# Kernel optimization log

Hardware: AMD Instinct MI355X
Metric: run time of the kernel (lower is better)

Reference implementation:

```python
import jax, jax.numpy as jnp
import numpy as np

N_NODES = 50000
N_EDGES = 500000
IN_FEATS = 64
H_FEATS = 128
NUM_CLASSES = 4
NUM_GRAPHS = 8
NODES_PER_GRAPH = N_NODES // NUM_GRAPHS


def setup_inputs() -> dict:
    key = jax.random.key(0)
    ks = jax.random.split(key, 12)
    in_feat = jax.random.normal(ks[0], (N_NODES, IN_FEATS), dtype=jnp.float32)
    e_weight = jax.random.uniform(ks[1], (N_EDGES,), dtype=jnp.float32)
    src = jax.random.randint(ks[2], (N_EDGES,), 0, N_NODES)
    dst = jax.random.randint(ks[3], (N_EDGES,), 0, N_NODES)
    batch_num_nodes = jnp.full((NUM_GRAPHS,), NODES_PER_GRAPH, dtype=jnp.int64)
    target_node = jax.random.randint(ks[4], (NUM_GRAPHS,), 0, NODES_PER_GRAPH)
    # Glorot-style init for GraphConv weights, zero bias (DGL defaults)
    def glorot(k, fan_in, fan_out):
        s = jnp.sqrt(6.0 / (fan_in + fan_out))
        return jax.random.uniform(k, (fan_in, fan_out), minval=-s, maxval=s, dtype=jnp.float32)
    W1 = glorot(ks[5], IN_FEATS, H_FEATS)
    b1 = jnp.zeros((H_FEATS,), dtype=jnp.float32)
    W2 = glorot(ks[6], H_FEATS, H_FEATS)
    b2 = jnp.zeros((H_FEATS,), dtype=jnp.float32)
    W3 = glorot(ks[7], H_FEATS, NUM_CLASSES)
    b3 = jnp.zeros((NUM_CLASSES,), dtype=jnp.float32)
    return {"in_feat": in_feat, "e_weight": e_weight, "src": src, "dst": dst,
            "batch_num_nodes": batch_num_nodes, "target_node": target_node,
            "W1": W1, "b1": b1, "W2": W2, "b2": b2, "W3": W3, "b3": b3}


def _graph_conv(h, src, dst, e_weight, W, b, out_norm, in_norm, n_nodes):
    # DGL GraphConv, norm='both', with per-edge weights:
    # h_src scaled by out_deg^-1/2, weighted sum over edges into dst,
    # scaled by in_deg^-1/2, then dense transform + bias.
    h = h * out_norm[:, None]
    msg = h[src] * e_weight[:, None]           # [E, d] gather + scale
    agg = jax.ops.segment_sum(msg, dst, num_segments=n_nodes)  # SPMM
    agg = agg * in_norm[:, None]
    return agg @ W + b


def reference(in_feat, e_weight, src, dst, batch_num_nodes, target_node,
              W1, b1, W2, b2, W3, b3):
    n = in_feat.shape[0]
    ones = jnp.ones((src.shape[0],), dtype=in_feat.dtype)
    out_deg = jnp.clip(jax.ops.segment_sum(ones, src, num_segments=n), 1.0)
    in_deg = jnp.clip(jax.ops.segment_sum(ones, dst, num_segments=n), 1.0)
    out_norm = jax.lax.rsqrt(out_deg)
    in_norm = jax.lax.rsqrt(in_deg)

    # target node offsets for batched graphs
    offsets = jnp.concatenate([jnp.zeros((1,), batch_num_nodes.dtype),
                               jnp.cumsum(batch_num_nodes)])[:-1]
    tgt = target_node + offsets

    h = jax.nn.relu(_graph_conv(in_feat, src, dst, e_weight, W1, b1, out_norm, in_norm, n))
    h = jax.nn.relu(_graph_conv(h, src, dst, e_weight, W2, b2, out_norm, in_norm, n))
    h = _graph_conv(h, src, dst, e_weight, W3, b3, out_norm, in_norm, n)
    return h[tgt]
```

## Files before the change

kernel.cpp:

```cpp
#include <hip/hip_runtime.h>

#define NND 50000
#define NED 500000
#define F0 64
#define F1 128
#define NCLS 4
#define NG 8

#define NBLK 256
#define NTHR 1024
#define EPT 2
#define TAILB 64
#define NBAR 6
#define NSUB 8
#define STG 2048
#define STGN 2048
#define BMW ((NND + 31) / 32)
#define EMASK 0x7FFFFu

#define N1CAP 4096
#define N2CAP 1024
#define E1CAP 32768
#define E2CAP 8192
#define E3CAP 2048


template <typename T>
__device__ __forceinline__ void st_wt(T* p, T v) {
    __hip_atomic_store(p, v, __ATOMIC_RELAXED, __HIP_MEMORY_SCOPE_AGENT);
}

__device__ __forceinline__ bool bt(const unsigned* __restrict__ bm, int n) {
    return (bm[n >> 5] >> (n & 31)) & 1u;
}
__device__ __forceinline__ bool bclaim(unsigned* bm, int n) {
    unsigned old = atomicOr(&bm[n >> 5], 1u << (n & 31));
    return !(old >> (n & 31) & 1u);
}
__device__ __forceinline__ void bset(unsigned* bm, int n) {
    atomicOr(&bm[n >> 5], 1u << (n & 31));
}

__device__ __forceinline__ void load_targets(const int* __restrict__ tnode,
                                             const unsigned* __restrict__ bnn,
                                             int* t) {
    bool is64 = true;
    #pragma unroll
    for (int k = 0; k < 4; k++) if (bnn[2 * k + 1] != 0u) { is64 = false; break; }
    long long off = 0;
    #pragma unroll
    for (int g = 0; g < NG; g++) {
        t[g] = tnode[g] + (int)off;
        off += is64 ? (long long)bnn[2 * g] : (long long)(int)bnn[g];
    }
}

__device__ __forceinline__ int tgt_of(int d, const int* t) {
    int g = -1;
    #pragma unroll
    for (int k = 0; k < NG; k++) if (d == t[k]) g = k;
    return g;
}

__device__ __forceinline__ void arrive(unsigned* bar, int i) {
    unsigned* sp = bar + (size_t)(i * (NSUB + 1) + (blockIdx.x & (NSUB - 1))) * 32;
    unsigned* mp = bar + (size_t)(i * (NSUB + 1) + NSUB) * 32;
    unsigned old = __hip_atomic_fetch_add(sp, 1u, __ATOMIC_RELAXED,
                                          __HIP_MEMORY_SCOPE_AGENT);
    if (old + 1u == (unsigned)(NBLK / NSUB))
        __hip_atomic_fetch_add(mp, 1u, __ATOMIC_RELAXED, __HIP_MEMORY_SCOPE_AGENT);
}
__device__ __forceinline__ void waitfull(unsigned* bar, int i) {
    unsigned* mp = bar + (size_t)(i * (NSUB + 1) + NSUB) * 32;
    while (__hip_atomic_load(mp, __ATOMIC_RELAXED, __HIP_MEMORY_SCOPE_AGENT)
           < (unsigned)NSUB)
        __builtin_amdgcn_s_sleep(1);
}
__device__ __forceinline__ void gbar(unsigned* bar, int i) {
    asm volatile("s_waitcnt vmcnt(0)" ::: "memory");
    __syncthreads();
    if (threadIdx.x == 0) { arrive(bar, i); waitfull(bar, i); }
    __syncthreads();
}
__device__ __forceinline__ void gbar_tail(unsigned* bar, int i) {
    asm volatile("s_waitcnt vmcnt(0)" ::: "memory");
    __syncthreads();
    if (threadIdx.x == 0) {
        unsigned* mp = bar + (size_t)(i * (NSUB + 1) + NSUB) * 32;
        __hip_atomic_fetch_add(mp, 1u, __ATOMIC_RELAXED, __HIP_MEMORY_SCOPE_AGENT);
        while (__hip_atomic_load(mp, __ATOMIC_RELAXED, __HIP_MEMORY_SCOPE_AGENT)
               < (unsigned)TAILB)
            __builtin_amdgcn_s_sleep(1);
    }
    __syncthreads();
}

__global__ __launch_bounds__(256) void k_init(char* ws, unsigned zw) {
    unsigned t = blockIdx.x * blockDim.x + threadIdx.x;
    if (t < zw) ((uint4*)ws)[t] = make_uint4(0u, 0u, 0u, 0u);
}

__global__ __launch_bounds__(NTHR) void k_main(
        const float* __restrict__ feat, const float* __restrict__ ew,
        const int* __restrict__ src, const int* __restrict__ dst,
        const int* __restrict__ tnode, const unsigned* __restrict__ bnn,
        const float* __restrict__ W1, const float* __restrict__ b1,
        const float* __restrict__ W2, const float* __restrict__ b2,
        const float* __restrict__ W3, const float* __restrict__ b3,
        float* out,
        int* idx1, int* idx2,
        unsigned* list1, unsigned* list2, unsigned* list3,
        unsigned* cnts, unsigned* incnt, unsigned* outcnt,
        unsigned* bm1, unsigned* bm2, unsigned* bmN,
        float* agg1c, float* agg2c, unsigned* bar,
        unsigned long long* zeroA, unsigned zaw) {
    __shared__ unsigned s_le, s_ln, s_eb, s_nb;
    __shared__ unsigned stage[STG];
    __shared__ int stageN[STGN];

    const int tid = threadIdx.x;
    const int gid = blockIdx.x * NTHR + tid;
    const int lane = tid & 63;
    int tg[NG]; load_targets(tnode, bnn, tg);

    {
        for (unsigned t = (unsigned)gid; t < zaw; t += NBLK * NTHR)
            st_wt(&zeroA[t], 0ULL);

        if (tid == 0) { s_le = 0; s_ln = 0; }
        __syncthreads();
        int base = gid * EPT;
        if (base < NED) {
            int2 d2 = *(const int2*)(dst + base);
            int dd[2] = {d2.x, d2.y};
            #pragma unroll
            for (int k = 0; k < 2; k++) {
                int d = dd[k];
                int g = tgt_of(d, tg);
                if (g >= 0) {
                    int e = base + k;
                    stage[atomicAdd(&s_le, 1u)] = ((unsigned)g << 19) | (unsigned)e;
                    int s = src[e];
                    bset(bmN, s);
                    if (bclaim(bm2, s)) stageN[atomicAdd(&s_ln, 1u)] = s;
                }
            }
        }
        __syncthreads();
        if (tid == 0) {
            s_eb = s_le ? atomicAdd(&cnts[4], s_le) : 0u;
            s_nb = s_ln ? atomicAdd(&cnts[1], s_ln) : 0u;
        }
        __syncthreads();
        for (unsigned t = tid; t < s_le; t += NTHR) {
            unsigned p = s_eb + t; if (p < E3CAP) st_wt(&list3[p], stage[t]);
        }
        for (unsigned t = tid; t < s_ln; t += NTHR) {
            int s = stageN[t]; unsigned id = s_nb + t;
            st_wt(&idx2[s], id < N2CAP ? (int)id : -1);
        }
        if (blockIdx.x == 0 && tid < NG * NCLS) st_wt(&out[tid], b3[tid & 3]);
    }
    gbar(bar, 0);

    {
        if (tid == 0) { s_le = 0; s_ln = 0; }
        __syncthreads();
        int base = gid * EPT;
        if (base < NED) {
            int2 d2 = *(const int2*)(dst + base);
            int dd[2] = {d2.x, d2.y};
            #pragma unroll
            for (int k = 0; k < 2; k++) {
                int d = dd[k];
                int g = tgt_of(d, tg);
                bool n2ok = false; int iv = -1;
                if (bt(bm2, d)) { iv = idx2[d]; n2ok = (unsigned)iv < N2CAP; }
                if (g >= 0 || n2ok) atomicAdd(&incnt[d], 1u);
                if (n2ok) {
                    int e = base + k;
                    stage[atomicAdd(&s_le, 1u)] = ((unsigned)iv << 19) | (unsigned)e;
                    int s = src[e];
                    bset(bmN, s);
                    if (bclaim(bm1, s)) stageN[atomicAdd(&s_ln, 1u)] = s;
                }
            }
        }
        __syncthreads();
        if (tid == 0) {
            s_eb = s_le ? atomicAdd(&cnts[3], s_le) : 0u;
            s_nb = s_ln ? atomicAdd(&cnts[0], s_ln) : 0u;
        }
        __syncthreads();
        for (unsigned t = tid; t < s_le; t += NTHR) {
            unsigned p = s_eb + t; if (p < E2CAP) st_wt(&list2[p], stage[t]);
        }
        for (unsigned t = tid; t < s_ln; t += NTHR) {
            int s = stageN[t]; unsigned id = s_nb + t;
            st_wt(&idx1[s], id < N1CAP ? (int)id : -1);
        }
    }
    gbar(bar, 1);

    {
        if (tid == 0) s_le = 0;
        __syncthreads();
        int base = gid * EPT;
        if (base < NED) {
            int2 d2 = *(const int2*)(dst + base);
            int dd[2] = {d2.x, d2.y};
            #pragma unroll
            for (int k = 0; k < 2; k++) {
                int d = dd[k];
                if (bt(bm1, d)) {
                    int iv = idx1[d];
                    if ((unsigned)iv < N1CAP) {
                        int e = base + k;
                        stage[atomicAdd(&s_le, 1u)] = ((unsigned)iv << 19) | (unsigned)e;
                        if (!bt(bm2, d) && tgt_of(d, tg) < 0) atomicAdd(&incnt[d], 1u);
                        bset(bmN, src[e]);
                    }
                }
            }
        }
        __syncthreads();
        if (tid == 0) s_eb = s_le ? atomicAdd(&cnts[2], s_le) : 0u;
        __syncthreads();
        for (unsigned t = tid; t < s_le; t += NTHR) {
            unsigned p = s_eb + t; if (p < E1CAP) st_wt(&list1[p], stage[t]);
        }
    }
    gbar(bar, 2);

    {
        int base = gid * EPT;
        if (base < NED) {
            int2 s2 = *(const int2*)(src + base);
            int ss[2] = {s2.x, s2.y};
            #pragma unroll
            for (int k = 0; k < 2; k++)
                if (bt(bmN, ss[k])) atomicAdd(&outcnt[ss[k]], 1u);
        }
    }
    gbar(bar, 3);

    {
        unsigned e1 = cnts[2]; if (e1 > E1CAP) e1 = E1CAP;
        unsigned w = (unsigned)gid >> 6;
        const unsigned nw = (NBLK * NTHR) >> 6;
        for (unsigned i = w; i < e1; i += 2 * nw) {
            unsigned pk0 = list1[i];
            unsigned j2 = i + nw;
            unsigned pk1 = (j2 < e1) ? list1[j2] : 0u;
            int e0 = pk0 & EMASK, i10 = pk0 >> 19;
            float we0 = ew[e0]; int s0 = src[e0];
            int e1i = pk1 & EMASK, i11 = pk1 >> 19;
            float we1 = 0.f; int s1 = 0;
            if (j2 < e1) { we1 = ew[e1i]; s1 = src[e1i]; }
            float wt0 = we0 * rsqrtf(fmaxf((float)outcnt[s0], 1.f));
            atomicAdd(&agg1c[(size_t)i10 * F0 + lane],
                      feat[(size_t)s0 * F0 + lane] * wt0);
            if (j2 < e1) {
                float wt1 = we1 * rsqrtf(fmaxf((float)outcnt[s1], 1.f));
                atomicAdd(&agg1c[(size_t)i11 * F0 + lane],
                          feat[(size_t)s1 * F0 + lane] * wt1);
            }
        }
    }
    {
        asm volatile("s_waitcnt vmcnt(0)" ::: "memory");
        __syncthreads();
        bool tail = blockIdx.x < TAILB;
        if (threadIdx.x == 0) {
            arrive(bar, 4);
            if (tail) waitfull(bar, 4);
        }
        if (!tail) return;
        __syncthreads();
    }

    {
        unsigned e2 = cnts[3]; if (e2 > E2CAP) e2 = E2CAP;
        unsigned w = (unsigned)gid >> 6;
        const unsigned nw = (TAILB * NTHR) >> 6;
        for (unsigned i = w; i < e2; i += nw) {
            unsigned pk = list2[i];
            int e = pk & EMASK, i2 = pk >> 19;
            float we = ew[e]; int s = src[e];
            unsigned i1 = (unsigned)idx1[s]; if (i1 >= N1CAP) continue;
            float wt = we * rsqrtf(fmaxf((float)outcnt[s], 1.f));
            float innorm1 = rsqrtf(fmaxf((float)incnt[s], 1.f));
            float rv = agg1c[(size_t)i1 * F0 + lane];
            float acc0 = 0.f, acc1 = 0.f;
            #pragma unroll 8
            for (int k2 = 0; k2 < F0; k2++) {
                float bv = __shfl(rv, k2, 64);
                acc0 += bv * W1[k2 * F1 + lane];
                acc1 += bv * W1[k2 * F1 + lane + 64];
            }
            float h0 = fmaxf(acc0 * innorm1 + b1[lane], 0.f) * wt;
            float h1v = fmaxf(acc1 * innorm1 + b1[lane + 64], 0.f) * wt;
            atomicAdd(&agg2c[(size_t)i2 * F1 + lane], h0);
            atomicAdd(&agg2c[(size_t)i2 * F1 + lane + 64], h1v);
        }
    }
    gbar_tail(bar, 5);

    {
        unsigned e3 = cnts[4]; if (e3 > E3CAP) e3 = E3CAP;
        unsigned w = (unsigned)gid >> 6;
        const unsigned nw = (TAILB * NTHR) >> 6;
        for (unsigned i = w; i < e3; i += nw) {
            unsigned pk = list3[i];
            int e = pk & EMASK, g = pk >> 19;
            float we = ew[e]; int s = src[e];
            unsigned i2 = (unsigned)idx2[s]; if (i2 >= N2CAP) continue;
            float wt = we * rsqrtf(fmaxf((float)outcnt[s], 1.f))
                          * rsqrtf(fmaxf((float)incnt[tg[g]], 1.f));
            float innorm2 = rsqrtf(fmaxf((float)incnt[s], 1.f));
            float rv0 = agg2c[(size_t)i2 * F1 + lane];
            float rv1 = agg2c[(size_t)i2 * F1 + lane + 64];
            float acc0 = 0.f, acc1 = 0.f;
            #pragma unroll 8
            for (int k2 = 0; k2 < 64; k2++) {
                float bv = __shfl(rv0, k2, 64);
                acc0 += bv * W2[k2 * F1 + lane];
                acc1 += bv * W2[k2 * F1 + lane + 64];
            }
            #pragma unroll 8
            for (int k2 = 0; k2 < 64; k2++) {
                float bv = __shfl(rv1, k2, 64);
                acc0 += bv * W2[(k2 + 64) * F1 + lane];
                acc1 += bv * W2[(k2 + 64) * F1 + lane + 64];
            }
            float h20 = fmaxf(acc0 * innorm2 + b2[lane], 0.f);
            float h21 = fmaxf(acc1 * innorm2 + b2[lane + 64], 0.f);
            float oc0 = (h20 * W3[lane * NCLS + 0] + h21 * W3[(lane + 64) * NCLS + 0]) * wt;
            float oc1 = (h20 * W3[lane * NCLS + 1] + h21 * W3[(lane + 64) * NCLS + 1]) * wt;
            float oc2 = (h20 * W3[lane * NCLS + 2] + h21 * W3[(lane + 64) * NCLS + 2]) * wt;
            float oc3 = (h20 * W3[lane * NCLS + 3] + h21 * W3[(lane + 64) * NCLS + 3]) * wt;
            #pragma unroll
            for (int off = 32; off; off >>= 1) {
                oc0 += __shfl_down(oc0, off, 64);
                oc1 += __shfl_down(oc1, off, 64);
                oc2 += __shfl_down(oc2, off, 64);
                oc3 += __shfl_down(oc3, off, 64);
            }
            if (lane == 0) {
                atomicAdd(&out[g * NCLS + 0], oc0);
                atomicAdd(&out[g * NCLS + 1], oc1);
                atomicAdd(&out[g * NCLS + 2], oc2);
                atomicAdd(&out[g * NCLS + 3], oc3);
            }
        }
    }
}

extern "C" void kernel_launch(void* const* d_in, const int* in_sizes, int n_in,
                              void* d_out, int out_size, void* d_ws, size_t ws_size,
                              hipStream_t stream) {
    const float* in_feat = (const float*)d_in[0];
    const float* ew      = (const float*)d_in[1];
    const int*   src     = (const int*)d_in[2];
    const int*   dst     = (const int*)d_in[3];
    const unsigned* bnn  = (const unsigned*)d_in[4];
    const int*   tnode   = (const int*)d_in[5];
    const float* W1 = (const float*)d_in[6];
    const float* b1 = (const float*)d_in[7];
    const float* W2 = (const float*)d_in[8];
    const float* b2 = (const float*)d_in[9];
    const float* W3 = (const float*)d_in[10];
    const float* b3 = (const float*)d_in[11];
    float* out = (float*)d_out;
    (void)in_sizes; (void)n_in; (void)out_size; (void)ws_size;

    char* ws = (char*)d_ws;
    size_t o = 0;
    auto alloc = [&](size_t bytes) { size_t r = o; o += (bytes + 255) & ~(size_t)255; return r; };

    size_t off_cnts = alloc(8 * 4);
    size_t off_bar  = alloc((size_t)NBAR * (NSUB + 1) * 32 * 4);
    size_t off_bm1  = alloc((size_t)BMW * 4);
    size_t off_bm2  = alloc((size_t)BMW * 4);
    size_t off_bmN  = alloc((size_t)BMW * 4);
    size_t init_bytes = o;
    size_t zeroA_start = o;
    size_t off_outcnt = alloc((size_t)NND * 4);
    size_t off_incnt  = alloc((size_t)NND * 4);
    size_t off_agg1   = alloc((size_t)N1CAP * F0 * 4);
    size_t off_agg2   = alloc((size_t)N2CAP * F1 * 4);
    size_t zeroA_bytes = o - zeroA_start;
    size_t off_idx2   = alloc((size_t)NND * 4);
    size_t off_idx1   = alloc((size_t)NND * 4);
    size_t off_list3  = alloc((size_t)E3CAP * 4);
    size_t off_list2  = alloc((size_t)E2CAP * 4);
    size_t off_list1  = alloc((size_t)E1CAP * 4);

    unsigned* cnts    = (unsigned*)(ws + off_cnts);
    unsigned* bar     = (unsigned*)(ws + off_bar);
    unsigned* bm1     = (unsigned*)(ws + off_bm1);
    unsigned* bm2     = (unsigned*)(ws + off_bm2);
    unsigned* bmN     = (unsigned*)(ws + off_bmN);
    unsigned* outcnt  = (unsigned*)(ws + off_outcnt);
    unsigned* incnt   = (unsigned*)(ws + off_incnt);
    float*    agg1c   = (float*)(ws + off_agg1);
    float*    agg2c   = (float*)(ws + off_agg2);
    int*      idx2    = (int*)(ws + off_idx2);
    int*      idx1    = (int*)(ws + off_idx1);
    unsigned* list3   = (unsigned*)(ws + off_list3);
    unsigned* list2   = (unsigned*)(ws + off_list2);
    unsigned* list1   = (unsigned*)(ws + off_list1);

    unsigned zw = (unsigned)(init_bytes / 16);
    k_init<<<(int)((zw + 255) / 256), 256, 0, stream>>>(ws, zw);

    k_main<<<NBLK, NTHR, 0, stream>>>(in_feat, ew, src, dst, tnode, bnn,
                                      W1, b1, W2, b2, W3, b3, out,
                                      idx1, idx2, list1, list2, list3,
                                      cnts, incnt, outcnt, bm1, bm2, bmN,
                                      agg1c, agg2c, bar,
                                      (unsigned long long*)(ws + zeroA_start),
                                      (unsigned)(zeroA_bytes / 8));
}
```

Before: 62.96 us.

## Compute full degrees up front and fuse layer-1 aggregation into frontier pass

Degree counting moves into the first pass: every edge atomically increments padded in/out count arrays (one counter per 32 bytes), which removes the bmN bitmap, the separate out-degree pass and its grid barrier. The layer-1 edge pass now runs the agg1 scatter straight from the block's shared-memory stage instead of writing list1 and waiting on another barrier, so two grid-wide barriers go away. In exchange there are a million global atomics over all edges rather than only frontier edges, and the padded count arrays (about 3.2 MB) are now zeroed by the init kernel rather than inside the main kernel.

```diff
diff --git a/kernel.cpp b/kernel.cpp
--- a/kernel.cpp
+++ b/kernel.cpp
@@ -6,12 +6,13 @@
 #define F1 128
 #define NCLS 4
 #define NG 8
+#define PAD 8
 
 #define NBLK 256
 #define NTHR 1024
 #define EPT 2
 #define TAILB 64
-#define NBAR 6
+#define NBAR 4
 #define NSUB 8
 #define STG 2048
 #define STGN 2048
@@ -20,7 +21,6 @@
 
 #define N1CAP 4096
 #define N2CAP 1024
-#define E1CAP 32768
 #define E2CAP 8192
 #define E3CAP 2048
 
@@ -36,9 +36,6 @@
 __device__ __forceinline__ bool bclaim(unsigned* bm, int n) {
     unsigned old = atomicOr(&bm[n >> 5], 1u << (n & 31));
     return !(old >> (n & 31) & 1u);
-}
-__device__ __forceinline__ void bset(unsigned* bm, int n) {
-    atomicOr(&bm[n >> 5], 1u << (n & 31));
 }
 
 __device__ __forceinline__ void load_targets(const int* __restrict__ tnode,
@@ -109,11 +106,10 @@
         const float* __restrict__ W3, const float* __restrict__ b3,
         float* out,
         int* idx1, int* idx2,
-        unsigned* list1, unsigned* list2, unsigned* list3,
-        unsigned* cnts, unsigned* incnt, unsigned* outcnt,
-        unsigned* bm1, unsigned* bm2, unsigned* bmN,
-        float* agg1c, float* agg2c, unsigned* bar,
-        unsigned long long* zeroA, unsigned zaw) {
+        unsigned* list2, unsigned* list3,
+        unsigned* cnts, unsigned* incntP, unsigned* outcntP,
+        unsigned* bm1, unsigned* bm2,
+        float* agg1c, float* agg2c, unsigned* bar) {
     __shared__ unsigned s_le, s_ln, s_eb, s_nb;
     __shared__ unsigned stage[STG];
     __shared__ int stageN[STGN];
@@ -124,9 +120,45 @@
     int tg[NG]; load_targets(tnode, bnn, tg);
 
     {
-        for (unsigned t = (unsigned)gid; t < zaw; t += NBLK * NTHR)
-            st_wt(&zeroA[t], 0ULL);
-
+        if (tid == 0) { s_le = 0; s_ln = 0; }
+        __syncthreads();
+        int base = gid * EPT;
+        if (base < NED) {
+            int2 d2 = *(const int2*)(dst + base);
+            int2 s2 = *(const int2*)(src + base);
+            int dd[2] = {d2.x, d2.y};
+            int ss[2] = {s2.x, s2.y};
+            #pragma unroll
+            for (int k = 0; k < 2; k++) {
+                int d = dd[k], s = ss[k];
+                atomicAdd(&incntP[(size_t)d * PAD], 1u);
+                atomicAdd(&outcntP[(size_t)s * PAD], 1u);
+                int g = tgt_of(d, tg);
+                if (g >= 0) {
+                    int e = base + k;
+                    stage[atomicAdd(&s_le, 1u)] = ((unsigned)g << 19) | (unsigned)e;
+                    if (bclaim(bm2, s)) stageN[atomicAdd(&s_ln, 1u)] = s;
+                }
+            }
+        }
+        __syncthreads();
+        if (tid == 0) {
+            s_eb = s_le ? atomicAdd(&cnts[4], s_le) : 0u;
+            s_nb = s_ln ? atomicAdd(&cnts[1], s_ln) : 0u;
+        }
+        __syncthreads();
+        for (unsigned t = tid; t < s_le; t += NTHR) {
+            unsigned p = s_eb + t; if (p < E3CAP) st_wt(&list3[p], stage[t]);
+        }
+        for (unsigned t = tid; t < s_ln; t += NTHR) {
+            int s = stageN[t]; unsigned id = s_nb + t;
+            st_wt(&idx2[s], id < N2CAP ? (int)id : -1);
+        }
+        if (blockIdx.x == 0 && tid < NG * NCLS) st_wt(&out[tid], b3[tid & 3]);
+    }
+    gbar(bar, 0);
+
+    {
         if (tid == 0) { s_le = 0; s_ln = 0; }
         __syncthreads();
         int base = gid * EPT;
@@ -136,53 +168,14 @@
             #pragma unroll
             for (int k = 0; k < 2; k++) {
                 int d = dd[k];
-                int g = tgt_of(d, tg);
-                if (g >= 0) {
-                    int e = base + k;
-                    stage[atomicAdd(&s_le, 1u)] = ((unsigned)g << 19) | (unsigned)e;
-                    int s = src[e];
-                    bset(bmN, s);
-                    if (bclaim(bm2, s)) stageN[atomicAdd(&s_ln, 1u)] = s;
-                }
-            }
-        }
-        __syncthreads();
-        if (tid == 0) {
-            s_eb = s_le ? atomicAdd(&cnts[4], s_le) : 0u;
-            s_nb = s_ln ? atomicAdd(&cnts[1], s_ln) : 0u;
-        }
-        __syncthreads();
-        for (unsigned t = tid; t < s_le; t += NTHR) {
-            unsigned p = s_eb + t; if (p < E3CAP) st_wt(&list3[p], stage[t]);
-        }
-        for (unsigned t = tid; t < s_ln; t += NTHR) {
-            int s = stageN[t]; unsigned id = s_nb + t;
-            st_wt(&idx2[s], id < N2CAP ? (int)id : -1);
-        }
-        if (blockIdx.x == 0 && tid < NG * NCLS) st_wt(&out[tid], b3[tid & 3]);
-    }
-    gbar(bar, 0);
-
-    {
-        if (tid == 0) { s_le = 0; s_ln = 0; }
-        __syncthreads();
-        int base = gid * EPT;
-        if (base < NED) {
-            int2 d2 = *(const int2*)(dst + base);
-            int dd[2] = {d2.x, d2.y};
-            #pragma unroll
-            for (int k = 0; k < 2; k++) {
-                int d = dd[k];
-                int g = tgt_of(d, tg);
-                bool n2ok = false; int iv = -1;
-                if (bt(bm2, d)) { iv = idx2[d]; n2ok = (unsigned)iv < N2CAP; }
-                if (g >= 0 || n2ok) atomicAdd(&incnt[d], 1u);
-                if (n2ok) {
-                    int e = base + k;
-                    stage[atomicAdd(&s_le, 1u)] = ((unsigned)iv << 19) | (unsigned)e;
-                    int s = src[e];
-                    bset(bmN, s);
-                    if (bclaim(bm1, s)) stageN[atomicAdd(&s_ln, 1u)] = s;
+                if (bt(bm2, d)) {
+                    int iv = idx2[d];
+                    if ((unsigned)iv < N2CAP) {
+                        int e = base + k;
+                        stage[atomicAdd(&s_le, 1u)] = ((unsigned)iv << 19) | (unsigned)e;
+                        int s = src[e];
+                        if (bclaim(bm1, s)) stageN[atomicAdd(&s_ln, 1u)] = s;
+                    }
                 }
             }
         }
@@ -214,57 +207,21 @@
                 int d = dd[k];
                 if (bt(bm1, d)) {
                     int iv = idx1[d];
-                    if ((unsigned)iv < N1CAP) {
-                        int e = base + k;
-                        stage[atomicAdd(&s_le, 1u)] = ((unsigned)iv << 19) | (unsigned)e;
-                        if (!bt(bm2, d) && tgt_of(d, tg) < 0) atomicAdd(&incnt[d], 1u);
-                        bset(bmN, src[e]);
-                    }
+                    if ((unsigned)iv < N1CAP)
+                        stage[atomicAdd(&s_le, 1u)] =
+                            ((unsigned)iv << 19) | (unsigned)(base + k);
                 }
             }
         }
         __syncthreads();
-        if (tid == 0) s_eb = s_le ? atomicAdd(&cnts[2], s_le) : 0u;
-        __syncthreads();
-        for (unsigned t = tid; t < s_le; t += NTHR) {
-            unsigned p = s_eb + t; if (p < E1CAP) st_wt(&list1[p], stage[t]);
-        }
-    }
-    gbar(bar, 2);
-
-    {
-        int base = gid * EPT;
-        if (base < NED) {
-            int2 s2 = *(const int2*)(src + base);
-            int ss[2] = {s2.x, s2.y};
-            #pragma unroll
-            for (int k = 0; k < 2; k++)
-                if (bt(bmN, ss[k])) atomicAdd(&outcnt[ss[k]], 1u);
-        }
-    }
-    gbar(bar, 3);
-
-    {
-        unsigned e1 = cnts[2]; if (e1 > E1CAP) e1 = E1CAP;
-        unsigned w = (unsigned)gid >> 6;
-        const unsigned nw = (NBLK * NTHR) >> 6;
-        for (unsigned i = w; i < e1; i += 2 * nw) {
-            unsigned pk0 = list1[i];
-            unsigned j2 = i + nw;
-            unsigned pk1 = (j2 < e1) ? list1[j2] : 0u;
-            int e0 = pk0 & EMASK, i10 = pk0 >> 19;
-            float we0 = ew[e0]; int s0 = src[e0];
-            int e1i = pk1 & EMASK, i11 = pk1 >> 19;
-            float we1 = 0.f; int s1 = 0;
-            if (j2 < e1) { we1 = ew[e1i]; s1 = src[e1i]; }
-            float wt0 = we0 * rsqrtf(fmaxf((float)outcnt[s0], 1.f));
-            atomicAdd(&agg1c[(size_t)i10 * F0 + lane],
-                      feat[(size_t)s0 * F0 + lane] * wt0);
-            if (j2 < e1) {
-                float wt1 = we1 * rsqrtf(fmaxf((float)outcnt[s1], 1.f));
-                atomicAdd(&agg1c[(size_t)i11 * F0 + lane],
-                          feat[(size_t)s1 * F0 + lane] * wt1);
-            }
+        unsigned cnt = s_le;
+        for (unsigned i = (unsigned)(tid >> 6); i < cnt; i += NTHR >> 6) {
+            unsigned pk = stage[i];
+            int e = pk & EMASK; unsigned i1 = pk >> 19;
+            int s = src[e];
+            float wt = ew[e] * rsqrtf(fmaxf((float)outcntP[(size_t)s * PAD], 1.f));
+            atomicAdd(&agg1c[(size_t)i1 * F0 + lane],
+                      feat[(size_t)s * F0 + lane] * wt);
         }
     }
     {
@@ -272,8 +229,8 @@
         __syncthreads();
         bool tail = blockIdx.x < TAILB;
         if (threadIdx.x == 0) {
-            arrive(bar, 4);
-            if (tail) waitfull(bar, 4);
+            arrive(bar, 2);
+            if (tail) waitfull(bar, 2);
         }
         if (!tail) return;
         __syncthreads();
@@ -288,8 +245,8 @@
             int e = pk & EMASK, i2 = pk >> 19;
             float we = ew[e]; int s = src[e];
             unsigned i1 = (unsigned)idx1[s]; if (i1 >= N1CAP) continue;
-            float wt = we * rsqrtf(fmaxf((float)outcnt[s], 1.f));
-            float innorm1 = rsqrtf(fmaxf((float)incnt[s], 1.f));
+            float wt = we * rsqrtf(fmaxf((float)outcntP[(size_t)s * PAD], 1.f));
+            float innorm1 = rsqrtf(fmaxf((float)incntP[(size_t)s * PAD], 1.f));
             float rv = agg1c[(size_t)i1 * F0 + lane];
             float acc0 = 0.f, acc1 = 0.f;
             #pragma unroll 8
@@ -304,7 +261,7 @@
             atomicAdd(&agg2c[(size_t)i2 * F1 + lane + 64], h1v);
         }
     }
-    gbar_tail(bar, 5);
+    gbar_tail(bar, 3);
 
     {
         unsigned e3 = cnts[4]; if (e3 > E3CAP) e3 = E3CAP;
@@ -315,9 +272,9 @@
             int e = pk & EMASK, g = pk >> 19;
             float we = ew[e]; int s = src[e];
             unsigned i2 = (unsigned)idx2[s]; if (i2 >= N2CAP) continue;
-            float wt = we * rsqrtf(fmaxf((float)outcnt[s], 1.f))
-                          * rsqrtf(fmaxf((float)incnt[tg[g]], 1.f));
-            float innorm2 = rsqrtf(fmaxf((float)incnt[s], 1.f));
+            float wt = we * rsqrtf(fmaxf((float)outcntP[(size_t)s * PAD], 1.f))
+                          * rsqrtf(fmaxf((float)incntP[(size_t)tg[g] * PAD], 1.f));
+            float innorm2 = rsqrtf(fmaxf((float)incntP[(size_t)s * PAD], 1.f));
             float rv0 = agg2c[(size_t)i2 * F1 + lane];
             float rv1 = agg2c[(size_t)i2 * F1 + lane + 64];
             float acc0 = 0.f, acc1 = 0.f;
@@ -378,47 +335,39 @@
     size_t o = 0;
     auto alloc = [&](size_t bytes) { size_t r = o; o += (bytes + 255) & ~(size_t)255; return r; };
 
-    size_t off_cnts = alloc(8 * 4);
-    size_t off_bar  = alloc((size_t)NBAR * (NSUB + 1) * 32 * 4);
-    size_t off_bm1  = alloc((size_t)BMW * 4);
-    size_t off_bm2  = alloc((size_t)BMW * 4);
-    size_t off_bmN  = alloc((size_t)BMW * 4);
+    size_t off_cnts  = alloc(8 * 4);
+    size_t off_bar   = alloc((size_t)NBAR * (NSUB + 1) * 32 * 4);
+    size_t off_bm1   = alloc((size_t)BMW * 4);
+    size_t off_bm2   = alloc((size_t)BMW * 4);
+    size_t off_inc   = alloc((size_t)NND * PAD * 4);
+    size_t off_outc  = alloc((size_t)NND * PAD * 4);
+    size_t off_agg1  = alloc((size_t)N1CAP * F0 * 4);
+    size_t off_agg2  = alloc((size_t)N2CAP * F1 * 4);
     size_t init_bytes = o;
-    size_t zeroA_start = o;
-    size_t off_outcnt = alloc((size_t)NND * 4);
-    size_t off_incnt  = alloc((size_t)NND * 4);
-    size_t off_agg1   = alloc((size_t)N1CAP * F0 * 4);
-    size_t off_agg2   = alloc((size_t)N2CAP * F1 * 4);
-    size_t zeroA_bytes = o - zeroA_start;
-    size_t off_idx2   = alloc((size_t)NND * 4);
-    size_t off_idx1   = alloc((size_t)NND * 4);
-    size_t off_list3  = alloc((size_t)E3CAP * 4);
-    size_t off_list2  = alloc((size_t)E2CAP * 4);
-    size_t off_list1  = alloc((size_t)E1CAP * 4);
+    size_t off_idx2  = alloc((size_t)NND * 4);
+    size_t off_idx1  = alloc((size_t)NND * 4);
+    size_t off_list3 = alloc((size_t)E3CAP * 4);
+    size_t off_list2 = alloc((size_t)E2CAP * 4);
 
     unsigned* cnts    = (unsigned*)(ws + off_cnts);
     unsigned* bar     = (unsigned*)(ws + off_bar);
     unsigned* bm1     = (unsigned*)(ws + off_bm1);
     unsigned* bm2     = (unsigned*)(ws + off_bm2);
-    unsigned* bmN     = (unsigned*)(ws + off_bmN);
-    unsigned* outcnt  = (unsigned*)(ws + off_outcnt);
-    unsigned* incnt   = (unsigned*)(ws + off_incnt);
+    unsigned* incntP  = (unsigned*)(ws + off_inc);
+    unsigned* outcntP = (unsigned*)(ws + off_outc);
     float*    agg1c   = (float*)(ws + off_agg1);
     float*    agg2c   = (float*)(ws + off_agg2);
     int*      idx2    = (int*)(ws + off_idx2);
     int*      idx1    = (int*)(ws + off_idx1);
     unsigned* list3   = (unsigned*)(ws + off_list3);
     unsigned* list2   = (unsigned*)(ws + off_list2);
-    unsigned* list1   = (unsigned*)(ws + off_list1);
 
     unsigned zw = (unsigned)(init_bytes / 16);
     k_init<<<(int)((zw + 255) / 256), 256, 0, stream>>>(ws, zw);
 
     k_main<<<NBLK, NTHR, 0, stream>>>(in_feat, ew, src, dst, tnode, bnn,
                                       W1, b1, W2, b2, W3, b3, out,
-                                      idx1, idx2, list1, list2, list3,
-                                      cnts, incnt, outcnt, bm1, bm2, bmN,
-                                      agg1c, agg2c, bar,
-                                      (unsigned long long*)(ws + zeroA_start),
-                                      (unsigned)(zeroA_bytes / 8));
-}
+                                      idx1, idx2, list2, list3,
+                                      cnts, incntP, outcntP, bm1, bm2,
+                                      agg1c, agg2c, bar);
+}
```

Result: slower. 86.12 us (+36.8%).

## Shrink to tail blocks before layer-1 aggregation and move zeroing into init kernel

Applied to the files above, without the earlier changes.

The partial-exit barrier now runs after the out-degree counting phase, so only TAILB blocks (raised to 128) do the layer-1 gather/atomic aggregation instead of all 256. Zeroing of the degree counters and aggregation buffers moves from the main kernel into the separate init kernel, and in-degree counting is restructured so targets count in phase 0 and second-hop nodes in phase 1. This is meant to cut main-kernel work and barrier waiting for blocks that have nothing left to do. The cost is a larger init kernel (about 1 MB of zeroing), and the layer-1 scatter now has fewer blocks to spread its work over.

```diff
diff --git a/kernel.cpp b/kernel.cpp
--- a/kernel.cpp
+++ b/kernel.cpp
@@ -10,7 +10,7 @@
 #define NBLK 256
 #define NTHR 1024
 #define EPT 2
-#define TAILB 64
+#define TAILB 128
 #define NBAR 6
 #define NSUB 8
 #define STG 2048
@@ -112,8 +112,7 @@
         unsigned* list1, unsigned* list2, unsigned* list3,
         unsigned* cnts, unsigned* incnt, unsigned* outcnt,
         unsigned* bm1, unsigned* bm2, unsigned* bmN,
-        float* agg1c, float* agg2c, unsigned* bar,
-        unsigned long long* zeroA, unsigned zaw) {
+        float* agg1c, float* agg2c, unsigned* bar) {
     __shared__ unsigned s_le, s_ln, s_eb, s_nb;
     __shared__ unsigned stage[STG];
     __shared__ int stageN[STGN];
@@ -124,9 +123,6 @@
     int tg[NG]; load_targets(tnode, bnn, tg);
 
     {
-        for (unsigned t = (unsigned)gid; t < zaw; t += NBLK * NTHR)
-            st_wt(&zeroA[t], 0ULL);
-
         if (tid == 0) { s_le = 0; s_ln = 0; }
         __syncthreads();
         int base = gid * EPT;
@@ -140,6 +136,7 @@
                 if (g >= 0) {
                     int e = base + k;
                     stage[atomicAdd(&s_le, 1u)] = ((unsigned)g << 19) | (unsigned)e;
+                    atomicAdd(&incnt[d], 1u);
                     int s = src[e];
                     bset(bmN, s);
                     if (bclaim(bm2, s)) stageN[atomicAdd(&s_ln, 1u)] = s;
@@ -173,16 +170,16 @@
             #pragma unroll
             for (int k = 0; k < 2; k++) {
                 int d = dd[k];
-                int g = tgt_of(d, tg);
-                bool n2ok = false; int iv = -1;
-                if (bt(bm2, d)) { iv = idx2[d]; n2ok = (unsigned)iv < N2CAP; }
-                if (g >= 0 || n2ok) atomicAdd(&incnt[d], 1u);
-                if (n2ok) {
-                    int e = base + k;
-                    stage[atomicAdd(&s_le, 1u)] = ((unsigned)iv << 19) | (unsigned)e;
-                    int s = src[e];
-                    bset(bmN, s);
-                    if (bclaim(bm1, s)) stageN[atomicAdd(&s_ln, 1u)] = s;
+                if (bt(bm2, d)) {
+                    int iv = idx2[d];
+                    if ((unsigned)iv < N2CAP) {
+                        int e = base + k;
+                        stage[atomicAdd(&s_le, 1u)] = ((unsigned)iv << 19) | (unsigned)e;
+                        if (tgt_of(d, tg) < 0) atomicAdd(&incnt[d], 1u);
+                        int s = src[e];
+                        bset(bmN, s);
+                        if (bclaim(bm1, s)) stageN[atomicAdd(&s_ln, 1u)] = s;
+                    }
                 }
             }
         }
@@ -241,20 +238,28 @@
             for (int k = 0; k < 2; k++)
                 if (bt(bmN, ss[k])) atomicAdd(&outcnt[ss[k]], 1u);
         }
-    }
-    gbar(bar, 3);
+        asm volatile("s_waitcnt vmcnt(0)" ::: "memory");
+        __syncthreads();
+        bool tail = blockIdx.x < TAILB;
+        if (threadIdx.x == 0) {
+            arrive(bar, 3);
+            if (tail) waitfull(bar, 3);
+        }
+        if (!tail) return;
+        __syncthreads();
+    }
 
     {
         unsigned e1 = cnts[2]; if (e1 > E1CAP) e1 = E1CAP;
         unsigned w = (unsigned)gid >> 6;
-        const unsigned nw = (NBLK * NTHR) >> 6;
+        const unsigned nw = (TAILB * NTHR) >> 6;
         for (unsigned i = w; i < e1; i += 2 * nw) {
             unsigned pk0 = list1[i];
             unsigned j2 = i + nw;
             unsigned pk1 = (j2 < e1) ? list1[j2] : 0u;
-            int e0 = pk0 & EMASK, i10 = pk0 >> 19;
+            int e0 = pk0 & EMASK; unsigned i10 = pk0 >> 19;
             float we0 = ew[e0]; int s0 = src[e0];
-            int e1i = pk1 & EMASK, i11 = pk1 >> 19;
+            int e1i = pk1 & EMASK; unsigned i11 = pk1 >> 19;
             float we1 = 0.f; int s1 = 0;
             if (j2 < e1) { we1 = ew[e1i]; s1 = src[e1i]; }
             float wt0 = we0 * rsqrtf(fmaxf((float)outcnt[s0], 1.f));
@@ -267,17 +272,7 @@
             }
         }
     }
-    {
-        asm volatile("s_waitcnt vmcnt(0)" ::: "memory");
-        __syncthreads();
-        bool tail = blockIdx.x < TAILB;
-        if (threadIdx.x == 0) {
-            arrive(bar, 4);
-            if (tail) waitfull(bar, 4);
-        }
-        if (!tail) return;
-        __syncthreads();
-    }
+    gbar_tail(bar, 4);
 
     {
         unsigned e2 = cnts[3]; if (e2 > E2CAP) e2 = E2CAP;
@@ -378,31 +373,29 @@
     size_t o = 0;
     auto alloc = [&](size_t bytes) { size_t r = o; o += (bytes + 255) & ~(size_t)255; return r; };
 
-    size_t off_cnts = alloc(8 * 4);
-    size_t off_bar  = alloc((size_t)NBAR * (NSUB + 1) * 32 * 4);
-    size_t off_bm1  = alloc((size_t)BMW * 4);
-    size_t off_bm2  = alloc((size_t)BMW * 4);
-    size_t off_bmN  = alloc((size_t)BMW * 4);
+    size_t off_cnts  = alloc(8 * 4);
+    size_t off_bar   = alloc((size_t)NBAR * (NSUB + 1) * 32 * 4);
+    size_t off_bm1   = alloc((size_t)BMW * 4);
+    size_t off_bm2   = alloc((size_t)BMW * 4);
+    size_t off_bmN   = alloc((size_t)BMW * 4);
+    size_t off_inc   = alloc((size_t)NND * 4);
+    size_t off_outc  = alloc((size_t)NND * 4);
+    size_t off_agg1  = alloc((size_t)N1CAP * F0 * 4);
+    size_t off_agg2  = alloc((size_t)N2CAP * F1 * 4);
     size_t init_bytes = o;
-    size_t zeroA_start = o;
-    size_t off_outcnt = alloc((size_t)NND * 4);
-    size_t off_incnt  = alloc((size_t)NND * 4);
-    size_t off_agg1   = alloc((size_t)N1CAP * F0 * 4);
-    size_t off_agg2   = alloc((size_t)N2CAP * F1 * 4);
-    size_t zeroA_bytes = o - zeroA_start;
-    size_t off_idx2   = alloc((size_t)NND * 4);
-    size_t off_idx1   = alloc((size_t)NND * 4);
-    size_t off_list3  = alloc((size_t)E3CAP * 4);
-    size_t off_list2  = alloc((size_t)E2CAP * 4);
-    size_t off_list1  = alloc((size_t)E1CAP * 4);
+    size_t off_idx2  = alloc((size_t)NND * 4);
+    size_t off_idx1  = alloc((size_t)NND * 4);
+    size_t off_list3 = alloc((size_t)E3CAP * 4);
+    size_t off_list2 = alloc((size_t)E2CAP * 4);
+    size_t off_list1 = alloc((size_t)E1CAP * 4);
 
     unsigned* cnts    = (unsigned*)(ws + off_cnts);
     unsigned* bar     = (unsigned*)(ws + off_bar);
     unsigned* bm1     = (unsigned*)(ws + off_bm1);
     unsigned* bm2     = (unsigned*)(ws + off_bm2);
     unsigned* bmN     = (unsigned*)(ws + off_bmN);
-    unsigned* outcnt  = (unsigned*)(ws + off_outcnt);
-    unsigned* incnt   = (unsigned*)(ws + off_incnt);
+    unsigned* incnt   = (unsigned*)(ws + off_inc);
+    unsigned* outcnt  = (unsigned*)(ws + off_outc);
     float*    agg1c   = (float*)(ws + off_agg1);
     float*    agg2c   = (float*)(ws + off_agg2);
     int*      idx2    = (int*)(ws + off_idx2);
@@ -418,7 +411,5 @@
                                       W1, b1, W2, b2, W3, b3, out,
                                       idx1, idx2, list1, list2, list3,
                                       cnts, incnt, outcnt, bm1, bm2, bmN,
-                                      agg1c, agg2c, bar,
-                                      (unsigned long long*)(ws + zeroA_start),
-                                      (unsigned)(zeroA_bytes / 8));
-}
+                                      agg1c, agg2c, bar);
+}
```

New measurement: 67.16 us. +6.7%, slower.
